# Performance work log

Hardware: AMD Instinct MI355X
Metric: run time of the kernel (lower is better)

The kernel has to match this reference:

```python
import jax, jax.numpy as jnp
import numpy as np

N = 100000   # nodes
E = 3200000  # edges (avg degree 32)
F_IN = 128   # node feature dim (lazy in_channels)
C = 16       # GAT out_channels, heads=1
ED = 2       # edge_dim
B = 512      # graphs in batch
OUT_X = 64; OUT_Y = 64; ROT = 4
EPS = 1e-5


def _bn(x, g, b):
    # BatchNorm1d in training mode: biased batch variance, eps=1e-5
    mu = x.mean(0, keepdims=True)
    var = x.var(0, keepdims=True)
    return g * (x - mu) * jax.lax.rsqrt(var + EPS) + b


def _gat(x, src, dst, edge_attr, W, We, att_s, att_d, att_e, bias):
    # PyG GATConv, heads=1: self-loops added with fill_value='mean' edge attrs
    n = x.shape[0]
    deg = jax.ops.segment_sum(jnp.ones_like(dst, jnp.float32), dst, num_segments=n)
    loop_attr = jax.ops.segment_sum(edge_attr, dst, num_segments=n) / jnp.maximum(deg, 1.0)[:, None]
    idx = jnp.arange(n)
    src_f = jnp.concatenate([src, idx])
    dst_f = jnp.concatenate([dst, idx])
    ea = jnp.concatenate([edge_attr, loop_attr], axis=0)  # [E+N, ED]
    h = x @ W                      # [N, C]
    a_s = h @ att_s                # [N]
    a_d = h @ att_d                # [N]
    a_e = (ea @ We) @ att_e        # [E+N]
    logits = jax.nn.leaky_relu(a_s[src_f] + a_d[dst_f] + a_e, 0.2)
    m = jax.ops.segment_max(logits, dst_f, num_segments=n)  # every node has a self-loop
    ex = jnp.exp(logits - m[dst_f])
    alpha = ex / jax.ops.segment_sum(ex, dst_f, num_segments=n)[dst_f]
    return jax.ops.segment_sum(alpha[:, None] * h[src_f], dst_f, num_segments=n) + bias


def _glorot(k, shp):
    lim = float(np.sqrt(6.0 / (shp[0] + shp[1])))
    return jax.random.uniform(k, shp, jnp.float32, -lim, lim)


def setup_inputs() -> dict:
    key = jax.random.key(0)
    k = jax.random.split(key, 48)
    d = {}
    d['x'] = jax.random.normal(k[0], (N, F_IN), jnp.float32)
    d['edge_index'] = jax.random.randint(k[1], (2, E), 0, N)
    d['edge_attr'] = jax.random.normal(k[2], (E, ED), jnp.float32)
    d['batch'] = jnp.sort(jax.random.randint(k[3], (N,), 0, B))
    # gat1
    d['W1'] = _glorot(k[4], (F_IN, C)); d['We1'] = _glorot(k[5], (ED, C))
    d['as1'] = 0.1 * jax.random.normal(k[6], (C,)); d['ad1'] = 0.1 * jax.random.normal(k[7], (C,))
    d['ae1'] = 0.1 * jax.random.normal(k[8], (C,)); d['b1'] = jnp.zeros((C,), jnp.float32)
    # norm1 (BatchNorm on nodes)
    d['g1'] = 1.0 + 0.1 * jax.random.normal(k[9], (C,)); d['bb1'] = 0.1 * jax.random.normal(k[10], (C,))
    # gat2
    d['W2'] = _glorot(k[11], (C, C)); d['We2'] = _glorot(k[12], (ED, C))
    d['as2'] = 0.1 * jax.random.normal(k[13], (C,)); d['ad2'] = 0.1 * jax.random.normal(k[14], (C,))
    d['ae2'] = 0.1 * jax.random.normal(k[15], (C,)); d['b2'] = jnp.zeros((C,), jnp.float32)
    # D2RL MLP tail
    d['gL1'] = 1.0 + 0.1 * jax.random.normal(k[16], (C,)); d['bL1'] = 0.1 * jax.random.normal(k[17], (C,))
    d['Wl1'] = _glorot(k[18], (C, C)); d['bl1'] = 0.1 * jax.random.normal(k[19], (C,))
    d['gL2'] = 1.0 + 0.1 * jax.random.normal(k[20], (2 * C,)); d['bL2'] = 0.1 * jax.random.normal(k[21], (2 * C,))
    d['Wl2'] = _glorot(k[22], (2 * C, C)); d['bl2'] = 0.1 * jax.random.normal(k[23], (C,))
    d['gL3'] = 1.0 + 0.1 * jax.random.normal(k[24], (2 * C,)); d['bL3'] = 0.1 * jax.random.normal(k[25], (2 * C,))
    d['Wl3'] = _glorot(k[26], (2 * C, C)); d['bl3'] = 0.1 * jax.random.normal(k[27], (C,))
    d['Wx'] = _glorot(k[28], (C, OUT_X)); d['bx'] = 0.1 * jax.random.normal(k[29], (OUT_X,))
    d['Wy'] = _glorot(k[30], (C, OUT_Y)); d['by'] = 0.1 * jax.random.normal(k[31], (OUT_Y,))
    d['Wr'] = _glorot(k[32], (C, ROT)); d['br'] = 0.1 * jax.random.normal(k[33], (ROT,))
    return d


def reference(x, edge_index, edge_attr, batch,
              W1, We1, as1, ad1, ae1, b1, g1, bb1,
              W2, We2, as2, ad2, ae2, b2,
              gL1, bL1, Wl1, bl1, gL2, bL2, Wl2, bl2, gL3, bL3, Wl3, bl3,
              Wx, bx, Wy, by, Wr, br):
    src, dst = edge_index[0], edge_index[1]
    h = jax.nn.relu(_gat(x, src, dst, edge_attr, W1, We1, as1, ad1, ae1, b1))
    h = _bn(h, g1, bb1)
    h = jax.nn.relu(_gat(h, src, dst, edge_attr, W2, We2, as2, ad2, ae2, b2))
    # MeanAggregation over graphs
    cnt = jax.ops.segment_sum(jnp.ones((h.shape[0],), jnp.float32), batch, num_segments=B)
    xe = jax.ops.segment_sum(h, batch, num_segments=B) / jnp.maximum(cnt, 1.0)[:, None]  # [B, C]
    z = _bn(xe, gL1, bL1)
    z = jax.nn.relu(z @ Wl1 + bl1)
    z = _bn(jnp.concatenate([z, xe], axis=1), gL2, bL2)
    z = jax.nn.relu(z @ Wl2 + bl2)
    z = _bn(jnp.concatenate([z, xe], axis=1), gL3, bL3)
    z = jax.nn.relu(z @ Wl3 + bl3)
    xx = jax.nn.softmax(z @ Wx + bx, axis=1)
    y = jax.nn.softmax(z @ Wy + by, axis=1)
    rot = jax.nn.softmax(z @ Wr + br, axis=1)
    return (xx, y, rot)
```

## Files before the change

### kernel.cpp

```cpp
#include <hip/hip_runtime.h>
#include <hip/hip_fp16.h>
#include <math.h>

#define C 16
#define FIN 128

__global__ __launch_bounds__(256) void k_gemm1(
    const float* __restrict__ x, const float* __restrict__ W,
    const float* __restrict__ asw, const float* __restrict__ adw,
    float* __restrict__ h, float* __restrict__ a_s, float* __restrict__ a_d, int n) {
  __shared__ float xs[64 * 129];
  __shared__ float Ws[FIN * C];
  __shared__ float pAs[4][64], pAd[4][64];
  int t = threadIdx.x;
  int node0 = blockIdx.x * 64;
  for (int i = t; i < FIN * C; i += 256) Ws[i] = W[i];
  for (int i = t; i < 64 * FIN; i += 256) {
    int r = i >> 7, c = i & 127;
    int node = node0 + r;
    xs[r * 129 + c] = (node < n) ? x[(size_t)node * FIN + c] : 0.f;
  }
  __syncthreads();
  int nn = t & 63, cg = (t >> 6) * 4, grp = t >> 6;
  float a0 = 0.f, a1 = 0.f, a2 = 0.f, a3 = 0.f;
  const float* xr = &xs[nn * 129];
  #pragma unroll 8
  for (int k = 0; k < FIN; ++k) {
    float xv = xr[k];
    const float* wr = &Ws[k * C + cg];
    a0 += xv * wr[0]; a1 += xv * wr[1]; a2 += xv * wr[2]; a3 += xv * wr[3];
  }
  int node = node0 + nn;
  if (node < n) {
    float4* outp = (float4*)&h[(size_t)node * C + cg];
    *outp = make_float4(a0, a1, a2, a3);
  }
  pAs[grp][nn] = a0 * asw[cg] + a1 * asw[cg + 1] + a2 * asw[cg + 2] + a3 * asw[cg + 3];
  pAd[grp][nn] = a0 * adw[cg] + a1 * adw[cg + 1] + a2 * adw[cg + 2] + a3 * adw[cg + 3];
  __syncthreads();
  if (t < 64 && node0 + t < n) {
    a_s[node0 + t] = pAs[0][t] + pAs[1][t] + pAs[2][t] + pAs[3][t];
    a_d[node0 + t] = pAd[0][t] + pAd[1][t] + pAd[2][t] + pAd[3][t];
  }
}

__global__ __launch_bounds__(256) void k_hist_rank(
    const int* __restrict__ dst, int* __restrict__ counts,
    int* __restrict__ rank, int ne) {
  int e = blockIdx.x * 256 + threadIdx.x;
  if (e < ne) rank[e] = atomicAdd(&counts[dst[e]], 1);
}

__global__ __launch_bounds__(512) void k_scan1(const int* __restrict__ counts,
                                               int* __restrict__ bsum, int n) {
  __shared__ int sd[512];
  int i = blockIdx.x * 512 + threadIdx.x;
  sd[threadIdx.x] = (i < n) ? counts[i] : 0;
  __syncthreads();
  for (int s = 256; s > 0; s >>= 1) {
    if (threadIdx.x < s) sd[threadIdx.x] += sd[threadIdx.x + s];
    __syncthreads();
  }
  if (threadIdx.x == 0) bsum[blockIdx.x] = sd[0];
}

__global__ __launch_bounds__(512) void k_scan2(int* __restrict__ bsum,
                                               int* __restrict__ offs,
                                               int nblk, int n) {
  __shared__ int sd[512];
  int t = threadIdx.x;
  int v = (t < nblk) ? bsum[t] : 0;
  sd[t] = v;
  __syncthreads();
  for (int off = 1; off < 512; off <<= 1) {
    int x = (t >= off) ? sd[t - off] : 0;
    __syncthreads();
    sd[t] += x;
    __syncthreads();
  }
  if (t < nblk) bsum[t] = sd[t] - v;
  if (t == nblk - 1) offs[n] = sd[t];
}

__global__ __launch_bounds__(512) void k_scan3(const int* __restrict__ counts,
                                               const int* __restrict__ bsum,
                                               int* __restrict__ offs, int n) {
  __shared__ int sd[512];
  int t = threadIdx.x;
  int i = blockIdx.x * 512 + t;
  int v = (i < n) ? counts[i] : 0;
  sd[t] = v;
  __syncthreads();
  for (int off = 1; off < 512; off <<= 1) {
    int x = (t >= off) ? sd[t - off] : 0;
    __syncthreads();
    sd[t] += x;
    __syncthreads();
  }
  if (i < n) offs[i] = bsum[blockIdx.x] + sd[t] - v;
}

__global__ __launch_bounds__(256) void k_scatter(
    const int* __restrict__ src, const int* __restrict__ dst,
    const float2* __restrict__ ea, const int* __restrict__ offs,
    const int* __restrict__ rank, uint2* __restrict__ bucket, int ne) {
  int e = blockIdx.x * 256 + threadIdx.x;
  if (e >= ne) return;
  int d = dst[e];
  float2 a = ea[e];
  __half2 hh = __floats2half2_rn(a.x, a.y);
  unsigned int hb;
  memcpy(&hb, &hh, 4);
  bucket[offs[d] + rank[e]] = make_uint2((unsigned int)src[e], hb);
}

__global__ __launch_bounds__(256) void k_gather(
    const uint2* __restrict__ bucket, const int* __restrict__ offs,
    const float* __restrict__ a_s, const float* __restrict__ a_d,
    const float* __restrict__ h,
    const float* __restrict__ We, const float* __restrict__ aew,
    const float* __restrict__ bias,
    float* __restrict__ outv, float* __restrict__ bnsum, float* __restrict__ bnsq,
    int do_bn, int n) {
  __shared__ float sbn[32];
  int t = threadIdx.x;
  if (t < 32) sbn[t] = 0.f;
  __syncthreads();

  int node = blockIdx.x * 16 + (t >> 4);
  int l = t & 15;
  float we0 = 0.f, we1 = 0.f;
  #pragma unroll
  for (int c = 0; c < C; ++c) { we0 += We[c] * aew[c]; we1 += We[C + c] * aew[c]; }

  float acc[C];
  #pragma unroll
  for (int c = 0; c < C; ++c) acc[c] = 0.f;
  float den = 0.f, lax = 0.f, lay = 0.f;
  int o0 = 0, o1 = 0;
  float adi = 0.f, asi = 0.f;
  if (node < n) {
    o0 = offs[node]; o1 = offs[node + 1];
    adi = a_d[node]; asi = a_s[node];
    for (int e = o0 + l; e < o1; e += 16) {
      uint2 r = bucket[e];
      int s = (int)r.x;
      __half2 hh;
      memcpy(&hh, &r.y, 4);
      float2 eaf = __half22float2(hh);
      float lg = a_s[s] + adi + eaf.x * we0 + eaf.y * we1;
      lg = lg > 0.f ? lg : 0.2f * lg;
      float ex = __expf(lg);
      den += ex; lax += eaf.x; lay += eaf.y;
      const float4* hp = (const float4*)&h[(size_t)s * C];
      float4 h0 = hp[0], h1 = hp[1], h2 = hp[2], h3 = hp[3];
      acc[0] += ex * h0.x; acc[1] += ex * h0.y; acc[2] += ex * h0.z; acc[3] += ex * h0.w;
      acc[4] += ex * h1.x; acc[5] += ex * h1.y; acc[6] += ex * h1.z; acc[7] += ex * h1.w;
      acc[8] += ex * h2.x; acc[9] += ex * h2.y; acc[10] += ex * h2.z; acc[11] += ex * h2.w;
      acc[12] += ex * h3.x; acc[13] += ex * h3.y; acc[14] += ex * h3.z; acc[15] += ex * h3.w;
    }
  }
  #pragma unroll
  for (int off = 1; off < 16; off <<= 1) {
    den += __shfl_xor(den, off);
    lax += __shfl_xor(lax, off);
    lay += __shfl_xor(lay, off);
    #pragma unroll
    for (int c = 0; c < C; ++c) acc[c] += __shfl_xor(acc[c], off);
  }

  float v = 0.f;
  if (node < n) {
    float dgc = fmaxf((float)(o1 - o0), 1.f);
    float lg = asi + adi + (lax * we0 + lay * we1) / dgc;
    lg = lg > 0.f ? lg : 0.2f * lg;
    float ex = __expf(lg);
    float hi = h[(size_t)node * C + l];
    float tot = acc[l] + ex * hi;
    den += ex;
    v = fmaxf(tot / den + bias[l], 0.f);
    outv[(size_t)node * C + l] = v;
  }
  if (do_bn) {
    float s = v, q = v * v;
    s += __shfl_down(s, 32); s += __shfl_down(s, 16);
    q += __shfl_down(q, 32); q += __shfl_down(q, 16);
    if ((t & 63) < 16) {
      atomicAdd(&sbn[l], s);
      atomicAdd(&sbn[16 + l], q);
    }
    __syncthreads();
    if (t < 16) atomicAdd(&bnsum[t], sbn[t]);
    else if (t < 32) atomicAdd(&bnsq[t - 16], sbn[t]);
  }
}

__global__ void k_bnp(const float* __restrict__ bnsum, const float* __restrict__ bnsq,
                      const float* __restrict__ g, const float* __restrict__ bb,
                      float* __restrict__ scale, float* __restrict__ shift, float invn) {
  int c = threadIdx.x;
  if (c >= C) return;
  float mean = bnsum[c] * invn;
  float var = bnsq[c] * invn - mean * mean;
  float s = g[c] * rsqrtf(var + 1e-5f);
  scale[c] = s; shift[c] = bb[c] - mean * s;
}

__global__ __launch_bounds__(256) void k_node2(
    const float* __restrict__ outv, const float* __restrict__ scale,
    const float* __restrict__ shift, const float* __restrict__ W2,
    const float* __restrict__ asw, const float* __restrict__ adw,
    float* __restrict__ h, float* __restrict__ a_s, float* __restrict__ a_d, int n) {
  __shared__ float w2s[C * C];
  if (threadIdx.x < C * C) w2s[threadIdx.x] = W2[threadIdx.x];
  __syncthreads();
  int i = blockIdx.x * 256 + threadIdx.x;
  if (i >= n) return;
  float hn[C];
  #pragma unroll
  for (int c = 0; c < C; ++c) hn[c] = outv[(size_t)i * C + c] * scale[c] + shift[c];
  float h2[C];
  #pragma unroll
  for (int j = 0; j < C; ++j) {
    float acc = 0.f;
    #pragma unroll
    for (int c = 0; c < C; ++c) acc += hn[c] * w2s[c * C + j];
    h2[j] = acc;
  }
  float hs = 0.f, hd = 0.f;
  #pragma unroll
  for (int j = 0; j < C; ++j) { hs += h2[j] * asw[j]; hd += h2[j] * adw[j]; }
  a_s[i] = hs; a_d[i] = hd;
  float4* hp = (float4*)&h[(size_t)i * C];
  hp[0] = make_float4(h2[0], h2[1], h2[2], h2[3]);
  hp[1] = make_float4(h2[4], h2[5], h2[6], h2[7]);
  hp[2] = make_float4(h2[8], h2[9], h2[10], h2[11]);
  hp[3] = make_float4(h2[12], h2[13], h2[14], h2[15]);
}

__global__ void k_gstart(const int* __restrict__ batch, int* __restrict__ gs,
                         int n, int B_) {
  int g = blockIdx.x * blockDim.x + threadIdx.x;
  if (g > B_) return;
  if (g == B_) { gs[B_] = n; return; }
  int lo = 0, hi = n;
  while (lo < hi) { int mid = (lo + hi) >> 1; if (batch[mid] < g) lo = mid + 1; else hi = mid; }
  gs[g] = lo;
}

__global__ __launch_bounds__(256) void k_xe(
    const float* __restrict__ outv, const int* __restrict__ gs,
    float* __restrict__ xe, int B_) {
  int wave = blockIdx.x * 4 + (threadIdx.x >> 6);
  if (wave >= B_) return;
  int lane = threadIdx.x & 63;
  int c = lane & 15, sub = lane >> 4;
  int base = gs[wave], end = gs[wave + 1];
  float s = 0.f;
  for (int n0 = base + sub; n0 < end; n0 += 4) s += outv[(size_t)n0 * C + c];
  s += __shfl_down(s, 32);
  s += __shfl_down(s, 16);
  if (lane < 16) xe[(size_t)wave * C + c] = s / fmaxf((float)(end - base), 1.f);
}

__global__ __launch_bounds__(512) void k_tail_z3(
    const float* __restrict__ xe_in,
    const float* __restrict__ gL1, const float* __restrict__ bL1,
    const float* __restrict__ Wl1, const float* __restrict__ bl1,
    const float* __restrict__ gL2, const float* __restrict__ bL2,
    const float* __restrict__ Wl2, const float* __restrict__ bl2,
    const float* __restrict__ gL3, const float* __restrict__ bL3,
    const float* __restrict__ Wl3, const float* __restrict__ bl3,
    float* __restrict__ z3buf, int B_) {
  __shared__ float ssum[2 * C], ssq[2 * C], sc[2 * C], sh[2 * C];
  int t = threadIdx.x;
  float invB = 1.f / (float)B_;
  float xe[C];
  #pragma unroll
  for (int c = 0; c < C; ++c) xe[c] = xe_in[(size_t)t * C + c];

  if (t < 2 * C) { ssum[t] = 0.f; ssq[t] = 0.f; }
  __syncthreads();
  #pragma unroll
  for (int c = 0; c < C; ++c) {
    float s = xe[c], q = xe[c] * xe[c];
    for (int o = 32; o > 0; o >>= 1) { s += __shfl_down(s, o); q += __shfl_down(q, o); }
    if ((t & 63) == 0) { atomicAdd(&ssum[c], s); atomicAdd(&ssq[c], q); }
  }
  __syncthreads();
  if (t < C) {
    float mean = ssum[t] * invB, var = ssq[t] * invB - mean * mean;
    float s = gL1[t] * rsqrtf(var + 1e-5f);
    sc[t] = s; sh[t] = bL1[t] - mean * s;
  }
  __syncthreads();
  float z[C];
  #pragma unroll
  for (int j = 0; j < C; ++j) {
    float acc = bl1[j];
    #pragma unroll
    for (int c = 0; c < C; ++c) acc += (xe[c] * sc[c] + sh[c]) * Wl1[c * C + j];
    z[j] = fmaxf(acc, 0.f);
  }
  __syncthreads();

  if (t < 2 * C) { ssum[t] = 0.f; ssq[t] = 0.f; }
  __syncthreads();
  #pragma unroll
  for (int c = 0; c < C; ++c) {
    float s = z[c], q = z[c] * z[c];
    for (int o = 32; o > 0; o >>= 1) { s += __shfl_down(s, o); q += __shfl_down(q, o); }
    if ((t & 63) == 0) { atomicAdd(&ssum[c], s); atomicAdd(&ssq[c], q); }
    float s2 = xe[c], q2 = xe[c] * xe[c];
    for (int o = 32; o > 0; o >>= 1) { s2 += __shfl_down(s2, o); q2 += __shfl_down(q2, o); }
    if ((t & 63) == 0) { atomicAdd(&ssum[C + c], s2); atomicAdd(&ssq[C + c], q2); }
  }
  __syncthreads();
  if (t < 2 * C) {
    float mean = ssum[t] * invB, var = ssq[t] * invB - mean * mean;
    float s = gL2[t] * rsqrtf(var + 1e-5f);
    sc[t] = s; sh[t] = bL2[t] - mean * s;
  }
  __syncthreads();
  float z2[C];
  #pragma unroll
  for (int j = 0; j < C; ++j) {
    float acc = bl2[j];
    #pragma unroll
    for (int c = 0; c < C; ++c) acc += (z[c] * sc[c] + sh[c]) * Wl2[c * C + j];
    #pragma unroll
    for (int c = 0; c < C; ++c) acc += (xe[c] * sc[C + c] + sh[C + c]) * Wl2[(C + c) * C + j];
    z2[j] = fmaxf(acc, 0.f);
  }
  __syncthreads();

  if (t < 2 * C) { ssum[t] = 0.f; ssq[t] = 0.f; }
  __syncthreads();
  #pragma unroll
  for (int c = 0; c < C; ++c) {
    float s = z2[c], q = z2[c] * z2[c];
    for (int o = 32; o > 0; o >>= 1) { s += __shfl_down(s, o); q += __shfl_down(q, o); }
    if ((t & 63) == 0) { atomicAdd(&ssum[c], s); atomicAdd(&ssq[c], q); }
    float s2 = xe[c], q2 = xe[c] * xe[c];
    for (int o = 32; o > 0; o >>= 1) { s2 += __shfl_down(s2, o); q2 += __shfl_down(q2, o); }
    if ((t & 63) == 0) { atomicAdd(&ssum[C + c], s2); atomicAdd(&ssq[C + c], q2); }
  }
  __syncthreads();
  if (t < 2 * C) {
    float mean = ssum[t] * invB, var = ssq[t] * invB - mean * mean;
    float s = gL3[t] * rsqrtf(var + 1e-5f);
    sc[t] = s; sh[t] = bL3[t] - mean * s;
  }
  __syncthreads();
  #pragma unroll
  for (int j = 0; j < C; ++j) {
    float acc = bl3[j];
    #pragma unroll
    for (int c = 0; c < C; ++c) acc += (z2[c] * sc[c] + sh[c]) * Wl3[c * C + j];
    #pragma unroll
    for (int c = 0; c < C; ++c) acc += (xe[c] * sc[C + c] + sh[C + c]) * Wl3[(C + c) * C + j];
    z3buf[(size_t)t * C + j] = fmaxf(acc, 0.f);
  }
}

__global__ __launch_bounds__(256) void k_heads(
    const float* __restrict__ z3buf,
    const float* __restrict__ Wx, const float* __restrict__ bx,
    const float* __restrict__ Wy, const float* __restrict__ by,
    const float* __restrict__ Wr, const float* __restrict__ br,
    float* __restrict__ out, int B_) {
  int wv = blockIdx.x * 4 + (threadIdx.x >> 6);
  if (wv >= B_) return;
  int lane = threadIdx.x & 63;
  float z[C];
  #pragma unroll
  for (int c = 0; c < C; ++c) z[c] = z3buf[(size_t)wv * C + c];

  float ax = bx[lane];
  #pragma unroll
  for (int c = 0; c < C; ++c) ax += z[c] * Wx[c * 64 + lane];
  float m = ax;
  #pragma unroll
  for (int o = 32; o > 0; o >>= 1) m = fmaxf(m, __shfl_xor(m, o));
  float e = __expf(ax - m);
  float s = e;
  #pragma unroll
  for (int o = 32; o > 0; o >>= 1) s += __shfl_xor(s, o);
  out[(size_t)wv * 64 + lane] = e / s;

  float ay = by[lane];
  #pragma unroll
  for (int c = 0; c < C; ++c) ay += z[c] * Wy[c * 64 + lane];
  m = ay;
  #pragma unroll
  for (int o = 32; o > 0; o >>= 1) m = fmaxf(m, __shfl_xor(m, o));
  e = __expf(ay - m);
  s = e;
  #pragma unroll
  for (int o = 32; o > 0; o >>= 1) s += __shfl_xor(s, o);
  out[(size_t)B_ * 64 + (size_t)wv * 64 + lane] = e / s;

  if (lane < 4) {
    float ar = br[lane];
    #pragma unroll
    for (int c = 0; c < C; ++c) ar += z[c] * Wr[c * 4 + lane];
    float mr = ar;
    mr = fmaxf(mr, __shfl_xor(mr, 1));
    mr = fmaxf(mr, __shfl_xor(mr, 2));
    float er = __expf(ar - mr);
    float sr = er;
    sr += __shfl_xor(sr, 1);
    sr += __shfl_xor(sr, 2);
    out[(size_t)B_ * 128 + (size_t)wv * 4 + lane] = er / sr;
  }
}

extern "C" void kernel_launch(void* const* d_in, const int* in_sizes, int n_in,
                              void* d_out, int out_size, void* d_ws, size_t ws_size,
                              hipStream_t stream) {
  const float* x     = (const float*)d_in[0];
  const int*   eidx  = (const int*)d_in[1];
  const float* eattr = (const float*)d_in[2];
  const int*   batch = (const int*)d_in[3];
  const float* W1  = (const float*)d_in[4];
  const float* We1 = (const float*)d_in[5];
  const float* as1 = (const float*)d_in[6];
  const float* ad1 = (const float*)d_in[7];
  const float* ae1 = (const float*)d_in[8];
  const float* b1  = (const float*)d_in[9];
  const float* g1  = (const float*)d_in[10];
  const float* bb1 = (const float*)d_in[11];
  const float* W2  = (const float*)d_in[12];
  const float* We2 = (const float*)d_in[13];
  const float* as2 = (const float*)d_in[14];
  const float* ad2 = (const float*)d_in[15];
  const float* ae2 = (const float*)d_in[16];
  const float* b2  = (const float*)d_in[17];
  const float* gL1 = (const float*)d_in[18];
  const float* bL1 = (const float*)d_in[19];
  const float* Wl1 = (const float*)d_in[20];
  const float* bl1 = (const float*)d_in[21];
  const float* gL2 = (const float*)d_in[22];
  const float* bL2 = (const float*)d_in[23];
  const float* Wl2 = (const float*)d_in[24];
  const float* bl2 = (const float*)d_in[25];
  const float* gL3 = (const float*)d_in[26];
  const float* bL3 = (const float*)d_in[27];
  const float* Wl3 = (const float*)d_in[28];
  const float* bl3 = (const float*)d_in[29];
  const float* Wx  = (const float*)d_in[30];
  const float* bx  = (const float*)d_in[31];
  const float* Wy  = (const float*)d_in[32];
  const float* by  = (const float*)d_in[33];
  const float* Wr  = (const float*)d_in[34];
  const float* br  = (const float*)d_in[35];

  int N = in_sizes[3];
  int E = in_sizes[2] / 2;
  int B = out_size / 132;
  int nblk = (N + 511) / 512;

  char* w = (char*)d_ws;
  size_t o = 0;
  auto alloc = [&](size_t bytes) { char* p = w + o; o += (bytes + 15) & ~15ull; return p; };
  uint2* bucket  = (uint2*)alloc((size_t)E * 8);
  int*   rank    = (int*)alloc((size_t)E * 4);
  float* h       = (float*)alloc((size_t)N * C * 4);
  float* outv    = (float*)alloc((size_t)N * C * 4);
  float* a_s     = (float*)alloc((size_t)N * 4);
  float* a_d     = (float*)alloc((size_t)N * 4);
  int*   counts  = (int*)alloc((size_t)N * 4);
  int*   offs    = (int*)alloc((size_t)(N + 4) * 4);
  int*   bsum    = (int*)alloc((size_t)(nblk + 4) * 4);
  float* bn      = (float*)alloc(64 * 4);
  float* xe      = (float*)alloc((size_t)B * C * 4);
  int*   gs      = (int*)alloc((size_t)(B + 4) * 4);
  float* z3buf   = (float*)alloc((size_t)B * C * 4);

  const int* src = eidx;
  const int* dst = eidx + E;
  int ebl = (E + 255) / 256;
  int nbl = (N + 255) / 256;

  hipMemsetAsync(counts, 0, (size_t)N * 4, stream);
  hipMemsetAsync(bn, 0, 32 * 4, stream);

  k_gemm1<<<(N + 63) / 64, 256, 0, stream>>>(x, W1, as1, ad1, h, a_s, a_d, N);
  k_hist_rank<<<ebl, 256, 0, stream>>>(dst, counts, rank, E);
  k_scan1<<<nblk, 512, 0, stream>>>(counts, bsum, N);
  k_scan2<<<1, 512, 0, stream>>>(bsum, offs, nblk, N);
  k_scan3<<<nblk, 512, 0, stream>>>(counts, bsum, offs, N);
  k_scatter<<<ebl, 256, 0, stream>>>(src, dst, (const float2*)eattr, offs, rank, bucket, E);
  k_gather<<<(N + 15) / 16, 256, 0, stream>>>(bucket, offs, a_s, a_d, h, We1, ae1, b1,
                                              outv, bn, bn + 16, 1, N);
  k_bnp<<<1, 64, 0, stream>>>(bn, bn + 16, g1, bb1, bn + 32, bn + 48, 1.f / (float)N);
  k_node2<<<nbl, 256, 0, stream>>>(outv, bn + 32, bn + 48, W2, as2, ad2, h, a_s, a_d, N);
  k_gather<<<(N + 15) / 16, 256, 0, stream>>>(bucket, offs, a_s, a_d, h, We2, ae2, b2,
                                              outv, bn, bn + 16, 0, N);
  k_gstart<<<(B + 1 + 255) / 256, 256, 0, stream>>>(batch, gs, N, B);
  k_xe<<<(B + 3) / 4, 256, 0, stream>>>(outv, gs, xe, B);
  k_tail_z3<<<1, B, 0, stream>>>(xe, gL1, bL1, Wl1, bl1, gL2, bL2, Wl2, bl2,
                                 gL3, bL3, Wl3, bl3, z3buf, B);
  k_heads<<<(B + 3) / 4, 256, 0, stream>>>(z3buf, Wx, bx, Wy, by, Wr, br,
                                           (float*)d_out, B);
}
```

Baseline: 783.8 us.

## Store node features h in fp16 and use 32 lanes per node in gather

The projected node features h are now written as fp16 by the GEMM and node2 kernels. The gather reads them as 32 bytes per source row instead of 64, which cuts the random-access gather traffic that dominates the edge aggregation. The gather also gives each node 32 lanes instead of 16, raising parallelism for edge iteration, and only the first 16 lanes write outputs. The cost is fp16 rounding of h before aggregation, plus an extra shuffle-reduction stage and idle lanes in the epilogue.

```diff
diff --git a/kernel.cpp b/kernel.cpp
--- a/kernel.cpp
+++ b/kernel.cpp
@@ -8,7 +8,7 @@
 __global__ __launch_bounds__(256) void k_gemm1(
     const float* __restrict__ x, const float* __restrict__ W,
     const float* __restrict__ asw, const float* __restrict__ adw,
-    float* __restrict__ h, float* __restrict__ a_s, float* __restrict__ a_d, int n) {
+    __half* __restrict__ h16, float* __restrict__ a_s, float* __restrict__ a_d, int n) {
   __shared__ float xs[64 * 129];
   __shared__ float Ws[FIN * C];
   __shared__ float pAs[4][64], pAd[4][64];
@@ -32,8 +32,10 @@
   }
   int node = node0 + nn;
   if (node < n) {
-    float4* outp = (float4*)&h[(size_t)node * C + cg];
-    *outp = make_float4(a0, a1, a2, a3);
+    __half2 p0 = __floats2half2_rn(a0, a1), p1 = __floats2half2_rn(a2, a3);
+    uint2 wv;
+    memcpy(&wv.x, &p0, 4); memcpy(&wv.y, &p1, 4);
+    *(uint2*)&h16[(size_t)node * C + cg] = wv;
   }
   pAs[grp][nn] = a0 * asw[cg] + a1 * asw[cg + 1] + a2 * asw[cg + 2] + a3 * asw[cg + 3];
   pAd[grp][nn] = a0 * adw[cg] + a1 * adw[cg + 1] + a2 * adw[cg + 2] + a3 * adw[cg + 3];
@@ -117,7 +119,7 @@
 __global__ __launch_bounds__(256) void k_gather(
     const uint2* __restrict__ bucket, const int* __restrict__ offs,
     const float* __restrict__ a_s, const float* __restrict__ a_d,
-    const float* __restrict__ h,
+    const __half* __restrict__ h16,
     const float* __restrict__ We, const float* __restrict__ aew,
     const float* __restrict__ bias,
     float* __restrict__ outv, float* __restrict__ bnsum, float* __restrict__ bnsq,
@@ -127,8 +129,8 @@
   if (t < 32) sbn[t] = 0.f;
   __syncthreads();
 
-  int node = blockIdx.x * 16 + (t >> 4);
-  int l = t & 15;
+  int node = blockIdx.x * 8 + (t >> 5);
+  int l = t & 31;
   float we0 = 0.f, we1 = 0.f;
   #pragma unroll
   for (int c = 0; c < C; ++c) { we0 += We[c] * aew[c]; we1 += We[C + c] * aew[c]; }
@@ -142,7 +144,7 @@
   if (node < n) {
     o0 = offs[node]; o1 = offs[node + 1];
     adi = a_d[node]; asi = a_s[node];
-    for (int e = o0 + l; e < o1; e += 16) {
+    for (int e = o0 + l; e < o1; e += 32) {
       uint2 r = bucket[e];
       int s = (int)r.x;
       __half2 hh;
@@ -152,16 +154,22 @@
       lg = lg > 0.f ? lg : 0.2f * lg;
       float ex = __expf(lg);
       den += ex; lax += eaf.x; lay += eaf.y;
-      const float4* hp = (const float4*)&h[(size_t)s * C];
-      float4 h0 = hp[0], h1 = hp[1], h2 = hp[2], h3 = hp[3];
-      acc[0] += ex * h0.x; acc[1] += ex * h0.y; acc[2] += ex * h0.z; acc[3] += ex * h0.w;
-      acc[4] += ex * h1.x; acc[5] += ex * h1.y; acc[6] += ex * h1.z; acc[7] += ex * h1.w;
-      acc[8] += ex * h2.x; acc[9] += ex * h2.y; acc[10] += ex * h2.z; acc[11] += ex * h2.w;
-      acc[12] += ex * h3.x; acc[13] += ex * h3.y; acc[14] += ex * h3.z; acc[15] += ex * h3.w;
+      const uint4* hp = (const uint4*)(h16 + (size_t)s * C);
+      union { uint4 u; __half2 p[4]; } U0, U1;
+      U0.u = hp[0]; U1.u = hp[1];
+      float2 f;
+      f = __half22float2(U0.p[0]); acc[0] += ex * f.x; acc[1] += ex * f.y;
+      f = __half22float2(U0.p[1]); acc[2] += ex * f.x; acc[3] += ex * f.y;
+      f = __half22float2(U0.p[2]); acc[4] += ex * f.x; acc[5] += ex * f.y;
+      f = __half22float2(U0.p[3]); acc[6] += ex * f.x; acc[7] += ex * f.y;
+      f = __half22float2(U1.p[0]); acc[8] += ex * f.x; acc[9] += ex * f.y;
+      f = __half22float2(U1.p[1]); acc[10] += ex * f.x; acc[11] += ex * f.y;
+      f = __half22float2(U1.p[2]); acc[12] += ex * f.x; acc[13] += ex * f.y;
+      f = __half22float2(U1.p[3]); acc[14] += ex * f.x; acc[15] += ex * f.y;
     }
   }
   #pragma unroll
-  for (int off = 1; off < 16; off <<= 1) {
+  for (int off = 1; off < 32; off <<= 1) {
     den += __shfl_xor(den, off);
     lax += __shfl_xor(lax, off);
     lay += __shfl_xor(lay, off);
@@ -170,12 +178,12 @@
   }
 
   float v = 0.f;
-  if (node < n) {
+  if (node < n && l < 16) {
     float dgc = fmaxf((float)(o1 - o0), 1.f);
     float lg = asi + adi + (lax * we0 + lay * we1) / dgc;
     lg = lg > 0.f ? lg : 0.2f * lg;
     float ex = __expf(lg);
-    float hi = h[(size_t)node * C + l];
+    float hi = __half2float(h16[(size_t)node * C + l]);
     float tot = acc[l] + ex * hi;
     den += ex;
     v = fmaxf(tot / den + bias[l], 0.f);
@@ -186,8 +194,8 @@
     s += __shfl_down(s, 32); s += __shfl_down(s, 16);
     q += __shfl_down(q, 32); q += __shfl_down(q, 16);
     if ((t & 63) < 16) {
-      atomicAdd(&sbn[l], s);
-      atomicAdd(&sbn[16 + l], q);
+      atomicAdd(&sbn[t & 15], s);
+      atomicAdd(&sbn[16 + (t & 15)], q);
     }
     __syncthreads();
     if (t < 16) atomicAdd(&bnsum[t], sbn[t]);
@@ -210,7 +218,7 @@
     const float* __restrict__ outv, const float* __restrict__ scale,
     const float* __restrict__ shift, const float* __restrict__ W2,
     const float* __restrict__ asw, const float* __restrict__ adw,
-    float* __restrict__ h, float* __restrict__ a_s, float* __restrict__ a_d, int n) {
+    __half* __restrict__ h16, float* __restrict__ a_s, float* __restrict__ a_d, int n) {
   __shared__ float w2s[C * C];
   if (threadIdx.x < C * C) w2s[threadIdx.x] = W2[threadIdx.x];
   __syncthreads();
@@ -231,11 +239,13 @@
   #pragma unroll
   for (int j = 0; j < C; ++j) { hs += h2[j] * asw[j]; hd += h2[j] * adw[j]; }
   a_s[i] = hs; a_d[i] = hd;
-  float4* hp = (float4*)&h[(size_t)i * C];
-  hp[0] = make_float4(h2[0], h2[1], h2[2], h2[3]);
-  hp[1] = make_float4(h2[4], h2[5], h2[6], h2[7]);
-  hp[2] = make_float4(h2[8], h2[9], h2[10], h2[11]);
-  hp[3] = make_float4(h2[12], h2[13], h2[14], h2[15]);
+  union { uint4 u; __half2 p[4]; } A, Bu;
+  A.p[0] = __floats2half2_rn(h2[0], h2[1]);  A.p[1] = __floats2half2_rn(h2[2], h2[3]);
+  A.p[2] = __floats2half2_rn(h2[4], h2[5]);  A.p[3] = __floats2half2_rn(h2[6], h2[7]);
+  Bu.p[0] = __floats2half2_rn(h2[8], h2[9]);  Bu.p[1] = __floats2half2_rn(h2[10], h2[11]);
+  Bu.p[2] = __floats2half2_rn(h2[12], h2[13]); Bu.p[3] = __floats2half2_rn(h2[14], h2[15]);
+  uint4* hp = (uint4*)(h16 + (size_t)i * C);
+  hp[0] = A.u; hp[1] = Bu.u;
 }
 
 __global__ void k_gstart(const int* __restrict__ batch, int* __restrict__ gs,
@@ -463,19 +473,19 @@
   char* w = (char*)d_ws;
   size_t o = 0;
   auto alloc = [&](size_t bytes) { char* p = w + o; o += (bytes + 15) & ~15ull; return p; };
-  uint2* bucket  = (uint2*)alloc((size_t)E * 8);
-  int*   rank    = (int*)alloc((size_t)E * 4);
-  float* h       = (float*)alloc((size_t)N * C * 4);
-  float* outv    = (float*)alloc((size_t)N * C * 4);
-  float* a_s     = (float*)alloc((size_t)N * 4);
-  float* a_d     = (float*)alloc((size_t)N * 4);
-  int*   counts  = (int*)alloc((size_t)N * 4);
-  int*   offs    = (int*)alloc((size_t)(N + 4) * 4);
-  int*   bsum    = (int*)alloc((size_t)(nblk + 4) * 4);
-  float* bn      = (float*)alloc(64 * 4);
-  float* xe      = (float*)alloc((size_t)B * C * 4);
-  int*   gs      = (int*)alloc((size_t)(B + 4) * 4);
-  float* z3buf   = (float*)alloc((size_t)B * C * 4);
+  uint2*  bucket = (uint2*)alloc((size_t)E * 8);
+  int*    rank   = (int*)alloc((size_t)E * 4);
+  __half* h16    = (__half*)alloc((size_t)N * C * 2);
+  float*  outv   = (float*)alloc((size_t)N * C * 4);
+  float*  a_s    = (float*)alloc((size_t)N * 4);
+  float*  a_d    = (float*)alloc((size_t)N * 4);
+  int*    counts = (int*)alloc((size_t)N * 4);
+  int*    offs   = (int*)alloc((size_t)(N + 4) * 4);
+  int*    bsum   = (int*)alloc((size_t)(nblk + 4) * 4);
+  float*  bn     = (float*)alloc(64 * 4);
+  float*  xe     = (float*)alloc((size_t)B * C * 4);
+  int*    gs     = (int*)alloc((size_t)(B + 4) * 4);
+  float*  z3buf  = (float*)alloc((size_t)B * C * 4);
 
   const int* src = eidx;
   const int* dst = eidx + E;
@@ -485,18 +495,18 @@
   hipMemsetAsync(counts, 0, (size_t)N * 4, stream);
   hipMemsetAsync(bn, 0, 32 * 4, stream);
 
-  k_gemm1<<<(N + 63) / 64, 256, 0, stream>>>(x, W1, as1, ad1, h, a_s, a_d, N);
+  k_gemm1<<<(N + 63) / 64, 256, 0, stream>>>(x, W1, as1, ad1, h16, a_s, a_d, N);
   k_hist_rank<<<ebl, 256, 0, stream>>>(dst, counts, rank, E);
   k_scan1<<<nblk, 512, 0, stream>>>(counts, bsum, N);
   k_scan2<<<1, 512, 0, stream>>>(bsum, offs, nblk, N);
   k_scan3<<<nblk, 512, 0, stream>>>(counts, bsum, offs, N);
   k_scatter<<<ebl, 256, 0, stream>>>(src, dst, (const float2*)eattr, offs, rank, bucket, E);
-  k_gather<<<(N + 15) / 16, 256, 0, stream>>>(bucket, offs, a_s, a_d, h, We1, ae1, b1,
-                                              outv, bn, bn + 16, 1, N);
+  k_gather<<<(N + 7) / 8, 256, 0, stream>>>(bucket, offs, a_s, a_d, h16, We1, ae1, b1,
+                                            outv, bn, bn + 16, 1, N);
   k_bnp<<<1, 64, 0, stream>>>(bn, bn + 16, g1, bb1, bn + 32, bn + 48, 1.f / (float)N);
-  k_node2<<<nbl, 256, 0, stream>>>(outv, bn + 32, bn + 48, W2, as2, ad2, h, a_s, a_d, N);
-  k_gather<<<(N + 15) / 16, 256, 0, stream>>>(bucket, offs, a_s, a_d, h, We2, ae2, b2,
-                                              outv, bn, bn + 16, 0, N);
+  k_node2<<<nbl, 256, 0, stream>>>(outv, bn + 32, bn + 48, W2, as2, ad2, h16, a_s, a_d, N);
+  k_gather<<<(N + 7) / 8, 256, 0, stream>>>(bucket, offs, a_s, a_d, h16, We2, ae2, b2,
+                                            outv, bn, bn + 16, 0, N);
   k_gstart<<<(B + 1 + 255) / 256, 256, 0, stream>>>(batch, gs, N, B);
   k_xe<<<(B + 3) / 4, 256, 0, stream>>>(outv, gs, xe, B);
   k_tail_z3<<<1, B, 0, stream>>>(xe, gL1, bL1, Wl1, bl1, gL2, bL2, Wl2, bl2,
```

After: 962.2 us. 22.8% more time.
